# Kernel optimization log

Measured on AMD Instinct MI355X. Metric: run time of the kernel, lower is better.

The kernel has to match this reference:

```python
import jax, jax.numpy as jnp
import numpy as np

B, NOP, NMA = 16, 512, 64
D_OP, D_MA, D_EG = 16, 8, 8
HID, OUT = 256, 128
NEG_SLOPE = 0.2


def _mlp(x, w1, b1, w2, b2, w3, b3):
    # Linear -> ELU -> Linear -> ELU -> Linear (MLPs.project)
    h = jax.nn.elu(x @ w1 + b1)
    h = jax.nn.elu(h @ w2 + b2)
    return h @ w3 + b3


def _gatop(op, ma, eg, ma_adj, pre_adj, sub_adj, attn_pre, params):
    # params: list of 5 tuples (w1,b1,w2,b2,w3,b3) for gnn_layers[0..4]
    num = op.shape[1]
    # flag_ma=0 aggregation: adj[...,None]*op[:,None,:,:] summed over dim -2 == adj @ op
    pre_f1 = _mlp(jnp.einsum('bij,bjd->bid', pre_adj, op), *params[1])   # [B,NOP,OUT]
    sub_f1 = _mlp(jnp.einsum('bij,bjd->bid', sub_adj, op), *params[2])   # [B,NOP,OUT]
    self_f1 = _mlp(op, *params[3])  # identity adjacency -> aggregation is op itself
    # machine-edge features: [B,NOP,NMA,D_MA+D_EG]
    ma_eg = jnp.concatenate([ma_adj[..., None] * ma[:, None, :, :], eg], axis=-1)
    # flag_ma=1: mask then per-pair MLP -> [B,NOP,NMA,OUT]
    ma_f1 = _mlp(ma_adj[..., None] * ma_eg, *params[0])
    # flag_ma=2: mean over machines counting nonzero entries
    cnt = jnp.sum(ma_f1 != 0.0, axis=-2).astype(ma_f1.dtype)
    ma_f2 = _mlp(jnp.sum(ma_f1, axis=-2) / cnt, *params[4])              # [B,NOP,OUT]
    # NOTE: original code uses attn_pre for ALL four scores (faithful)
    att = lambda f: jnp.sum(f * attn_pre, axis=-1, keepdims=True)        # [B,NOP,1]
    pre_ut, sub_ut, self_ut, ma_ut = att(pre_f1), att(sub_f1), att(self_f1), att(ma_f2)
    lrelu = lambda x: jax.nn.leaky_relu(x, NEG_SLOPE)
    scores = jnp.concatenate([
        lrelu(pre_ut + self_ut), lrelu(sub_ut + self_ut),
        lrelu(self_ut + self_ut), lrelu(ma_ut + self_ut)], axis=1)       # [B,4*NOP,1]
    alpha = jax.nn.softmax(scores, axis=1)
    a_pre = alpha[:, :num]
    a_sub = alpha[:, num:2 * num]
    a_self = alpha[:, 2 * num:3 * num]
    a_ma = alpha[:, 3 * num:]
    return jax.nn.sigmoid(a_pre * pre_f1 + a_sub * sub_f1 + a_self * self_f1 + a_ma * ma_f2)


def setup_inputs() -> dict:
    key = jax.random.key(0)
    ks = jax.random.split(key, 40)
    inp = {
        'op': jax.random.normal(ks[0], (B, NOP, D_OP), jnp.float32),
        'ma': jax.random.normal(ks[1], (B, NMA, D_MA), jnp.float32),
        'eg': jax.random.normal(ks[2], (B, NOP, NMA, D_EG), jnp.float32),
        'op_ma_adj': jax.random.randint(ks[3], (B, NOP, NMA), 0, 2, jnp.int32),
        'op_pre_adj': jax.random.randint(ks[4], (B, NOP, NOP), 0, 2, jnp.int32),
        'op_sub_adj': jax.random.randint(ks[5], (B, NOP, NOP), 0, 2, jnp.int32),
        'batch_idxes': jnp.arange(B, dtype=jnp.int32),
        'attn_pre': jax.random.normal(ks[6], (1, 1, OUT), jnp.float32) * 0.1,
    }
    ins = [D_MA + D_EG, D_OP, D_OP, D_OP, OUT]
    k = 7
    for i, din in enumerate(ins):
        inp[f'm{i}_w1'] = jax.random.normal(ks[k], (din, HID), jnp.float32) / np.sqrt(din); k += 1
        inp[f'm{i}_b1'] = jnp.zeros((HID,), jnp.float32)
        inp[f'm{i}_w2'] = jax.random.normal(ks[k], (HID, HID), jnp.float32) / np.sqrt(HID); k += 1
        inp[f'm{i}_b2'] = jnp.zeros((HID,), jnp.float32)
        inp[f'm{i}_w3'] = jax.random.normal(ks[k], (HID, OUT), jnp.float32) / np.sqrt(HID); k += 1
        inp[f'm{i}_b3'] = jnp.zeros((OUT,), jnp.float32)
    return inp


def reference(op, ma, eg, op_ma_adj, op_pre_adj, op_sub_adj, batch_idxes, attn_pre,
              m0_w1, m0_b1, m0_w2, m0_b2, m0_w3, m0_b3,
              m1_w1, m1_b1, m1_w2, m1_b2, m1_w3, m1_b3,
              m2_w1, m2_b1, m2_w2, m2_b2, m2_w3, m2_b3,
              m3_w1, m3_b1, m3_w2, m3_b2, m3_w3, m3_b3,
              m4_w1, m4_b1, m4_w2, m4_b2, m4_w3, m4_b3):
    ma_adj = op_ma_adj[batch_idxes].astype(op.dtype)
    pre_adj = op_pre_adj[batch_idxes].astype(op.dtype)
    sub_adj = op_sub_adj[batch_idxes].astype(op.dtype)
    params = [
        (m0_w1, m0_b1, m0_w2, m0_b2, m0_w3, m0_b3),
        (m1_w1, m1_b1, m1_w2, m1_b2, m1_w3, m1_b3),
        (m2_w1, m2_b1, m2_w2, m2_b2, m2_w3, m2_b3),
        (m3_w1, m3_b1, m3_w2, m3_b2, m3_w3, m3_b3),
        (m4_w1, m4_b1, m4_w2, m4_b2, m4_w3, m4_b3),
    ]
    return _gatop(op, ma, eg, ma_adj, pre_adj, sub_adj, attn_pre, params)
```

## Files before the change

kernel.cpp:

```cpp
#include <hip/hip_runtime.h>
#include <math.h>

#define NBb  16
#define NOPc 512
#define NMAc 64
#define HIDc 256
#define OUTc 128
#define NROW (NBb * NOPc)
#define NEMAX (NROW * NMAc)

#define HX(row, col) ((col) ^ (8 * ((row) & 15)))
#define FX(row, col) ((col) ^ (4 * ((row) & 15)))

typedef unsigned int uint32;
typedef unsigned short ush;
typedef __attribute__((ext_vector_type(8))) short bf16x8;
typedef __attribute__((ext_vector_type(4))) float f32x4;

__device__ __forceinline__ ush f2bf(float v) {
    uint32 u = __float_as_uint(v);
    u += 0x7FFFu + ((u >> 16) & 1u);
    return (ush)(u >> 16);
}
__device__ __forceinline__ float bf2f(ush b) { return __uint_as_float(((uint32)b) << 16); }
__device__ __forceinline__ float eluf(float x) { return x > 0.f ? x : expm1f(x); }
__device__ __forceinline__ float eluf_fast(float x) { return x > 0.f ? x : __expf(x) - 1.f; }
__device__ __forceinline__ uint32 pkbf(float a, float b) {
    return __builtin_amdgcn_perm(__float_as_uint(b), __float_as_uint(a), 0x07060302u);
}
__device__ __forceinline__ uint32 pkbf_rne(float a, float b) {
    return (uint32)f2bf(a) | ((uint32)f2bf(b) << 16);
}
__device__ __forceinline__ void split2(float a, float b, uint32& hp, uint32& lp) {
    const uint32 ua = __float_as_uint(a), ub = __float_as_uint(b);
    hp = __builtin_amdgcn_perm(ub, ua, 0x07060302u);
    const float ra = a - __uint_as_float(ua & 0xFFFF0000u);
    const float rb = b - __uint_as_float(ub & 0xFFFF0000u);
    lp = __builtin_amdgcn_perm(__float_as_uint(rb), __float_as_uint(ra), 0x07060302u);
}
__device__ __forceinline__ uint32 pkadj(int a, int b) {
    return (a ? 0x3F80u : 0u) | (b ? 0x3F800000u : 0u);
}

#define MFMA(A, B, C) __builtin_amdgcn_mfma_f32_16x16x32_bf16((A), (B), (C), 0, 0, 0)

struct MlpPack {
    const ush *w1h, *w1l, *w2h, *w2l, *w3h, *w3l;
    const float *b1, *b2, *b3;
};

__device__ __forceinline__ void mlp3_core32(
    const MlpPack& P, const int KB1,
    const ush* Xh, const ush* Xl, ush* Hh, ush* Hl, f32x4 acc3[2][2])
{
    const int tid = threadIdx.x;
    const int wv = tid >> 6, lane = tid & 63, r = lane & 15, g = lane >> 4;
    const int KX = KB1 * 32;

    {
        f32x4 acc[4][2];
        #pragma unroll
        for (int a = 0; a < 4; ++a) {
            const float4 bv = *(const float4*)(P.b1 + (wv * 4 + a) * 16 + 4 * g);
            #pragma unroll
            for (int m = 0; m < 2; ++m) acc[a][m] = f32x4{bv.x, bv.y, bv.z, bv.w};
        }
        #pragma unroll 1
        for (int kb = 0; kb < KB1; ++kb) {
            bf16x8 wh[4], wl[4];
            #pragma unroll
            for (int a = 0; a < 4; ++a) {
                const size_t o = ((size_t)(kb * 16 + (wv * 4 + a)) * 64 + lane) * 8;
                wh[a] = *(const bf16x8*)(P.w1h + o);
                wl[a] = *(const bf16x8*)(P.w1l + o);
            }
            #pragma unroll
            for (int m = 0; m < 2; ++m) {
                const int row = 16 * m + r;
                const int ki = kb * 32 + 8 * g;
                bf16x8 xh = *(const bf16x8*)(Xh + row * KX + ki);
                bf16x8 xl = *(const bf16x8*)(Xl + row * KX + ki);
                #pragma unroll
                for (int a = 0; a < 4; ++a) {
                    acc[a][m] = MFMA(wh[a], xh, acc[a][m]);
                    acc[a][m] = MFMA(wh[a], xl, acc[a][m]);
                    acc[a][m] = MFMA(wl[a], xh, acc[a][m]);
                }
            }
        }
        #pragma unroll
        for (int a = 0; a < 4; ++a) {
            const int n0 = (wv * 4 + a) * 16 + 4 * g;
            #pragma unroll
            for (int m = 0; m < 2; ++m) {
                const int row = 16 * m + r;
                const float y0 = eluf_fast(acc[a][m][0]);
                const float y1 = eluf_fast(acc[a][m][1]);
                const float y2 = eluf_fast(acc[a][m][2]);
                const float y3 = eluf_fast(acc[a][m][3]);
                uint2 uh, ul;
                split2(y0, y1, uh.x, ul.x);
                split2(y2, y3, uh.y, ul.y);
                const int idx = row * 256 + HX(row, n0);
                *(uint2*)(Hh + idx) = uh;
                *(uint2*)(Hl + idx) = ul;
            }
        }
    }
    __syncthreads();

    {
        f32x4 acc[4][2];
        #pragma unroll
        for (int a = 0; a < 4; ++a) {
            const float4 bv = *(const float4*)(P.b2 + (wv * 4 + a) * 16 + 4 * g);
            #pragma unroll
            for (int m = 0; m < 2; ++m) acc[a][m] = f32x4{bv.x, bv.y, bv.z, bv.w};
        }
        #pragma unroll 1
        for (int kb = 0; kb < 8; ++kb) {
            bf16x8 wh[4], wl[4];
            #pragma unroll
            for (int a = 0; a < 4; ++a) {
                const size_t o = ((size_t)(kb * 16 + (wv * 4 + a)) * 64 + lane) * 8;
                wh[a] = *(const bf16x8*)(P.w2h + o);
                wl[a] = *(const bf16x8*)(P.w2l + o);
            }
            #pragma unroll
            for (int m = 0; m < 2; ++m) {
                const int row = 16 * m + r;
                const int k0 = kb * 32 + 8 * g;
                const int idx = row * 256 + HX(row, k0);
                bf16x8 hh = *(const bf16x8*)(Hh + idx);
                bf16x8 hl = *(const bf16x8*)(Hl + idx);
                #pragma unroll
                for (int a = 0; a < 4; ++a) {
                    acc[a][m] = MFMA(wh[a], hh, acc[a][m]);
                    acc[a][m] = MFMA(wh[a], hl, acc[a][m]);
                    acc[a][m] = MFMA(wl[a], hh, acc[a][m]);
                }
            }
        }
        __syncthreads();
        #pragma unroll
        for (int a = 0; a < 4; ++a) {
            const int n0 = (wv * 4 + a) * 16 + 4 * g;
            #pragma unroll
            for (int m = 0; m < 2; ++m) {
                const int row = 16 * m + r;
                const float y0 = eluf_fast(acc[a][m][0]);
                const float y1 = eluf_fast(acc[a][m][1]);
                const float y2 = eluf_fast(acc[a][m][2]);
                const float y3 = eluf_fast(acc[a][m][3]);
                uint2 uh, ul;
                split2(y0, y1, uh.x, ul.x);
                split2(y2, y3, uh.y, ul.y);
                const int idx = row * 256 + HX(row, n0);
                *(uint2*)(Hh + idx) = uh;
                *(uint2*)(Hl + idx) = ul;
            }
        }
    }
    __syncthreads();

    {
        #pragma unroll
        for (int a = 0; a < 2; ++a) {
            const float4 bv = *(const float4*)(P.b3 + (wv * 2 + a) * 16 + 4 * g);
            #pragma unroll
            for (int m = 0; m < 2; ++m) acc3[a][m] = f32x4{bv.x, bv.y, bv.z, bv.w};
        }
        #pragma unroll 1
        for (int kb = 0; kb < 8; ++kb) {
            bf16x8 wh[2], wl[2];
            #pragma unroll
            for (int a = 0; a < 2; ++a) {
                const size_t o = ((size_t)(kb * 8 + (wv * 2 + a)) * 64 + lane) * 8;
                wh[a] = *(const bf16x8*)(P.w3h + o);
                wl[a] = *(const bf16x8*)(P.w3l + o);
            }
            #pragma unroll
            for (int m = 0; m < 2; ++m) {
                const int row = 16 * m + r;
                const int k0 = kb * 32 + 8 * g;
                const int idx = row * 256 + HX(row, k0);
                bf16x8 hh = *(const bf16x8*)(Hh + idx);
                bf16x8 hl = *(const bf16x8*)(Hl + idx);
                #pragma unroll
                for (int a = 0; a < 2; ++a) {
                    acc3[a][m] = MFMA(wh[a], hh, acc3[a][m]);
                    acc3[a][m] = MFMA(wh[a], hl, acc3[a][m]);
                    acc3[a][m] = MFMA(wl[a], hh, acc3[a][m]);
                }
            }
        }
    }
}

__global__ __launch_bounds__(256) void count_kernel(const int* __restrict__ ma_adj,
                                                    const int* __restrict__ bidx,
                                                    int* __restrict__ counts)
{
    const int tid = threadIdx.x;
    const int rid = blockIdx.x * 4 + (tid >> 6);
    const int lane = tid & 63;
    const int b = rid >> 9, i = rid & 511;
    const int bi = bidx[b];
    const int active = (ma_adj[((size_t)bi * NOPc + i) * NMAc + lane] != 0) ? 1 : 0;
    const unsigned long long mk = __ballot(active);
    if (lane == 0) counts[rid] = (int)__popcll(mk);
}

__global__ __launch_bounds__(1024) void scan_kernel(const int* __restrict__ counts,
                                                    int* __restrict__ bases,
                                                    int* __restrict__ natot,
                                                    ush* __restrict__ Xq,
                                                    ush* __restrict__ rowseg)
{
    __shared__ int tot[1024];
    const int t = threadIdx.x;
    int loc[8];
    int s = 0;
    #pragma unroll
    for (int k = 0; k < 8; ++k) { loc[k] = s; s += counts[t * 8 + k]; }
    tot[t] = s;
    __syncthreads();
    for (int off = 1; off < 1024; off <<= 1) {
        const int v = (t >= off) ? tot[t - off] : 0;
        __syncthreads();
        tot[t] += v;
        __syncthreads();
    }
    const int base = tot[t] - s;
    #pragma unroll
    for (int k = 0; k < 8; ++k) bases[t * 8 + k] = base + loc[k];
    const int NA = tot[1023];
    if (t == 0) *natot = NA;
    __syncthreads();
    const int NApad = (NA + 63) & ~63;
    for (int idx = NA * 16 + t; idx < NApad * 16; idx += 1024) Xq[idx] = 0;
    for (int idx = NA + t; idx < NApad; idx += 1024) rowseg[idx] = (ush)0xFFFFu;
}

struct PackDesc { const float* src; ush* dh; ush* dl; int kreal; int kbn; int nbn; };
struct PrepArgs {
    PackDesc d[15];
    const float* op; const int* pre_adj; const int* sub_adj; const int* ma_adj;
    const int* bidx;
    float* pre_agg; float* sub_agg;
    const float *z_b1, *z_w2, *z_b2, *z_w3, *z_b3;
    float* f1z;
    const float* ma; const float* eg; const int* bases;
    ush* Xq; ush* rowseg; float* sumG;
};

__global__ __launch_bounds__(256) void prep_kernel(PrepArgs A)
{
    __shared__ float shmem[8192];
    const int blk = blockIdx.x;
    const int t = threadIdx.x;
    if (blk < 960) {
        const PackDesc d = A.d[blk >> 6];
        const int sub = blk & 63;
        const int total = d.kbn * d.nbn * 512;
        const int N = d.nbn * 16;
        for (int idx = sub * 256 + t; idx < total; idx += 64 * 256) {
            const int e = idx & 7;
            const int l = (idx >> 3) & 63;
            const int t2 = idx >> 9;
            const int nb = t2 % d.nbn;
            const int kb = t2 / d.nbn;
            const int k = kb * 32 + ((l >> 4) << 3) + e;
            const int n = nb * 16 + (l & 15);
            const float v = (k < d.kreal) ? d.src[(size_t)k * N + n] : 0.f;
            const ush hi = f2bf(v);
            d.dh[idx] = hi;
            d.dl[idx] = f2bf(v - bf2f(hi));
        }
    } else if (blk < 1088) {
        const int e = blk - 960;
        const int b = e >> 3;
        const int i0 = (e & 7) * 64;
        const int bi = A.bidx[b];
        ush* opH = (ush*)shmem;
        ush* opL = opH + 8192;
        for (int idx = t; idx < 8192; idx += 256) {
            const int j = idx >> 4, dd = idx & 15;
            const float v = A.op[(size_t)b * 8192 + idx];
            const int kb = j >> 5, gg = (j >> 3) & 3, ee = j & 7;
            const int di = ((kb * 64 + gg * 16 + dd) << 3) + ee;
            const uint32 uv = __float_as_uint(v);
            opH[di] = (ush)(uv >> 16);
            const float rest = v - __uint_as_float(uv & 0xFFFF0000u);
            opL[di] = (ush)(__float_as_uint(rest) >> 16);
        }
        __syncthreads();
        const int wv = t >> 6, lane = t & 63, r = lane & 15, g = lane >> 4;
        const int i = i0 + wv * 16 + r;
        const int4* pr4 = (const int4*)(A.pre_adj + ((size_t)bi * NOPc + i) * NOPc);
        const int4* sr4 = (const int4*)(A.sub_adj + ((size_t)bi * NOPc + i) * NOPc);
        f32x4 accP = {0.f, 0.f, 0.f, 0.f}, accS = {0.f, 0.f, 0.f, 0.f};
        #pragma unroll 2
        for (int kb = 0; kb < 16; ++kb) {
            const int jo = kb * 8 + 2 * g;
            const int4 p0 = pr4[jo], p1 = pr4[jo + 1];
            const int4 s0 = sr4[jo], s1 = sr4[jo + 1];
            bf16x8 ap, as;
            {
                uint32 u0 = pkadj(p0.x, p0.y), u1 = pkadj(p0.z, p0.w);
                uint32 u2 = pkadj(p1.x, p1.y), u3 = pkadj(p1.z, p1.w);
                uint32* pa = (uint32*)&ap;
                pa[0] = u0; pa[1] = u1; pa[2] = u2; pa[3] = u3;
            }
            {
                uint32 u0 = pkadj(s0.x, s0.y), u1 = pkadj(s0.z, s0.w);
                uint32 u2 = pkadj(s1.x, s1.y), u3 = pkadj(s1.z, s1.w);
                uint32* pa = (uint32*)&as;
                pa[0] = u0; pa[1] = u1; pa[2] = u2; pa[3] = u3;
            }
            const bf16x8 oh = *(const bf16x8*)(opH + ((kb * 64 + lane) << 3));
            const bf16x8 ol = *(const bf16x8*)(opL + ((kb * 64 + lane) << 3));
            accP = MFMA(oh, ap, accP);
            accP = MFMA(ol, ap, accP);
            accS = MFMA(oh, as, accS);
            accS = MFMA(ol, as, accS);
        }
        float4 vp, vs;
        vp.x = accP[0]; vp.y = accP[1]; vp.z = accP[2]; vp.w = accP[3];
        vs.x = accS[0]; vs.y = accS[1]; vs.z = accS[2]; vs.w = accS[3];
        *(float4*)&A.pre_agg[((size_t)b * NOPc + i) * 16 + 4 * g] = vp;
        *(float4*)&A.sub_agg[((size_t)b * NOPc + i) * 16 + 4 * g] = vs;
    } else if (blk == 1088) {
        shmem[t] = eluf(A.z_b1[t]);
        __syncthreads();
        float acc = A.z_b2[t];
        for (int k = 0; k < 256; ++k) acc += shmem[k] * A.z_w2[(size_t)k * 256 + t];
        __syncthreads();
        shmem[256 + t] = eluf(acc);
        __syncthreads();
        if (t < 128) {
            float a = A.z_b3[t];
            for (int k = 0; k < 256; ++k) a += shmem[256 + k] * A.z_w3[(size_t)k * 128 + t];
            A.f1z[t] = a;
        }
    } else {
        const int rid = (blk - 1089) * 4 + (t >> 6);
        const int lane = t & 63;
        const int b = rid >> 9, i = rid & 511;
        const int bi = A.bidx[b];
        const int act = (A.ma_adj[((size_t)bi * NOPc + i) * NMAc + lane] != 0) ? 1 : 0;
        const unsigned long long mk = __ballot(act);
        if (act) {
            const int pos = A.bases[rid] + (int)__popcll(mk & ((1ull << lane) - 1ull));
            const float4* mp = (const float4*)(A.ma + ((size_t)b * NMAc + lane) * 8);
            const float4* ep = (const float4*)(A.eg + (((size_t)b * NOPc + i) * NMAc + lane) * 8);
            const float4 m0 = mp[0], m1 = mp[1], e0 = ep[0], e1 = ep[1];
            uint4 u0, u1;
            u0.x = pkbf_rne(m0.x, m0.y); u0.y = pkbf_rne(m0.z, m0.w);
            u0.z = pkbf_rne(m1.x, m1.y); u0.w = pkbf_rne(m1.z, m1.w);
            u1.x = pkbf_rne(e0.x, e0.y); u1.y = pkbf_rne(e0.z, e0.w);
            u1.z = pkbf_rne(e1.x, e1.y); u1.w = pkbf_rne(e1.z, e1.w);
            uint4* dst = (uint4*)(A.Xq + (size_t)pos * 16);
            dst[0] = u0;
            dst[1] = u1;
            A.rowseg[pos] = (ush)rid;
        }
        A.sumG[(size_t)rid * 128 + lane] = 0.f;
        A.sumG[(size_t)rid * 128 + 64 + lane] = 0.f;
    }
}

struct EF1Args {
    const ush* Xq; const ush* rowseg; const int* natot; MlpPack P0;
    float* sumG;
    const float* X[3]; MlpPack P[3]; float* f1[3]; float* ut[3];
};

__global__ __launch_bounds__(256, 4) void edge_f1_kernel(EF1Args A, const float* __restrict__ attn)
{
    __shared__ unsigned char smem[36992];
    const int blk = blockIdx.x;
    const int tid = threadIdx.x;
    const int wv = tid >> 6, lane = tid & 63, r = lane & 15, g = lane >> 4;

    if (blk < 8192) {
        const int NA = *A.natot;
        const int tile = blk;
        if (tile * 64 >= NA) return;
        ush* Hh = (ush*)smem;
        ush* segid = (ush*)(smem + 32768);
        const MlpPack& P = A.P0;
        if (tid < 64) segid[tid] = A.rowseg[(size_t)tile * 64 + tid];

        {
            f32x4 acc[4][4];
            #pragma unroll
            for (int a = 0; a < 4; ++a) {
                const float4 bv = *(const float4*)(P.b1 + (wv * 4 + a) * 16 + 4 * g);
                #pragma unroll
                for (int m = 0; m < 4; ++m) acc[a][m] = f32x4{bv.x, bv.y, bv.z, bv.w};
            }
            bf16x8 wh[4];
            #pragma unroll
            for (int a = 0; a < 4; ++a)
                wh[a] = *(const bf16x8*)(P.w1h + ((size_t)(wv * 4 + a) * 64 + lane) * 8);
            #pragma unroll
            for (int m = 0; m < 4; ++m) {
                const int gr = tile * 64 + 16 * m + r;
                bf16x8 xh = {0, 0, 0, 0, 0, 0, 0, 0};
                if (g < 2) xh = *(const bf16x8*)(A.Xq + (size_t)gr * 16 + 8 * g);
                #pragma unroll
                for (int a = 0; a < 4; ++a) acc[a][m] = MFMA(wh[a], xh, acc[a][m]);
            }
            #pragma unroll
            for (int a = 0; a < 4; ++a) {
                const int n0 = (wv * 4 + a) * 16 + 4 * g;
                #pragma unroll
                for (int m = 0; m < 4; ++m) {
                    const int row = 16 * m + r;
                    const float y0 = eluf_fast(acc[a][m][0]);
                    const float y1 = eluf_fast(acc[a][m][1]);
                    const float y2 = eluf_fast(acc[a][m][2]);
                    const float y3 = eluf_fast(acc[a][m][3]);
                    uint2 u; u.x = pkbf(y0, y1); u.y = pkbf(y2, y3);
                    *(uint2*)(Hh + row * 256 + HX(row, n0)) = u;
                }
            }
        }
        __syncthreads();

        {
            f32x4 acc[4][4];
            #pragma unroll
            for (int a = 0; a < 4; ++a) {
                const float4 bv = *(const float4*)(P.b2 + (wv * 4 + a) * 16 + 4 * g);
                #pragma unroll
                for (int m = 0; m < 4; ++m) acc[a][m] = f32x4{bv.x, bv.y, bv.z, bv.w};
            }
            #pragma unroll 1
            for (int kb = 0; kb < 8; ++kb) {
                bf16x8 wh[4];
                #pragma unroll
                for (int a = 0; a < 4; ++a)
                    wh[a] = *(const bf16x8*)(P.w2h + ((size_t)(kb * 16 + (wv * 4 + a)) * 64 + lane) * 8);
                #pragma unroll
                for (int m = 0; m < 4; ++m) {
                    const int row = 16 * m + r;
                    const int k0 = kb * 32 + 8 * g;
                    bf16x8 hh = *(const bf16x8*)(Hh + row * 256 + HX(row, k0));
                    #pragma unroll
                    for (int a = 0; a < 4; ++a) acc[a][m] = MFMA(wh[a], hh, acc[a][m]);
                }
            }
            __syncthreads();
            #pragma unroll
            for (int a = 0; a < 4; ++a) {
                const int n0 = (wv * 4 + a) * 16 + 4 * g;
                #pragma unroll
                for (int m = 0; m < 4; ++m) {
                    const int row = 16 * m + r;
                    const float y0 = eluf_fast(acc[a][m][0]);
                    const float y1 = eluf_fast(acc[a][m][1]);
                    const float y2 = eluf_fast(acc[a][m][2]);
                    const float y3 = eluf_fast(acc[a][m][3]);
                    uint2 u; u.x = pkbf(y0, y1); u.y = pkbf(y2, y3);
                    *(uint2*)(Hh + row * 256 + HX(row, n0)) = u;
                }
            }
        }
        __syncthreads();

        f32x4 acc3[2][4];
        #pragma unroll
        for (int a = 0; a < 2; ++a) {
            const float4 bv = *(const float4*)(P.b3 + (wv * 2 + a) * 16 + 4 * g);
            #pragma unroll
            for (int m = 0; m < 4; ++m) acc3[a][m] = f32x4{bv.x, bv.y, bv.z, bv.w};
        }
        #pragma unroll 1
        for (int kb = 0; kb < 8; ++kb) {
            bf16x8 wh[2];
            #pragma unroll
            for (int a = 0; a < 2; ++a)
                wh[a] = *(const bf16x8*)(P.w3h + ((size_t)(kb * 8 + (wv * 2 + a)) * 64 + lane) * 8);
            #pragma unroll
            for (int m = 0; m < 4; ++m) {
                const int row = 16 * m + r;
                const int k0 = kb * 32 + 8 * g;
                bf16x8 hh = *(const bf16x8*)(Hh + row * 256 + HX(row, k0));
                #pragma unroll
                for (int a = 0; a < 2; ++a) acc3[a][m] = MFMA(wh[a], hh, acc3[a][m]);
            }
        }
        __syncthreads();

        float* f1buf = (float*)Hh;
        #pragma unroll
        for (int a = 0; a < 2; ++a) {
            const int n0 = (wv * 2 + a) * 16 + 4 * g;
            #pragma unroll
            for (int m = 0; m < 4; ++m) {
                const int row = 16 * m + r;
                float4 y;
                y.x = acc3[a][m][0];
                y.y = acc3[a][m][1];
                y.z = acc3[a][m][2];
                y.w = acc3[a][m][3];
                *(float4*)&f1buf[row * 128 + FX(row, n0)] = y;
            }
        }
        __syncthreads();

        {
            const int c = tid & 127, h = tid >> 7;
            const int r0p = h * 32;
            float accS = 0.f;
            int cur = -1;
            #pragma unroll
            for (int j = 0; j < 32; ++j) {
                const int rl = r0p + j;
                const int sg = (int)segid[rl];
                if (sg != cur) {
                    if ((unsigned)cur < (unsigned)NROW)
                        atomicAdd(&A.sumG[(size_t)cur * 128 + c], accS);
                    cur = sg; accS = 0.f;
                }
                accS += f1buf[rl * 128 + FX(rl, c)];
            }
            if ((unsigned)cur < (unsigned)NROW)
                atomicAdd(&A.sumG[(size_t)cur * 128 + c], accS);
        }
    } else {
        const int pb = blk - 8192;
        const int p = pb >> 8;
        const int row0 = (pb & 255) * 32;
        ush* Xh = (ush*)smem;
        ush* Xl = (ush*)(smem + 2048);
        ush* Hh = (ush*)(smem + 4096);
        ush* Hl = (ush*)(smem + 20480);
        float* UT = (float*)(smem + 36864);
        const float* Xg = A.X[p];
        const MlpPack P = A.P[p];
        float* f1_out = A.f1[p];
        float* ut_out = A.ut[p];
        if (tid < 32) UT[tid] = 0.f;
        for (int idx = tid; idx < 32 * 32; idx += 256) {
            const int row = idx >> 5, k = idx & 31;
            float v = 0.f;
            if (k < 16) v = Xg[(size_t)(row0 + row) * 16 + k];
            const uint32 uv = __float_as_uint(v);
            Xh[idx] = (ush)(uv >> 16);
            const float rest = v - __uint_as_float(uv & 0xFFFF0000u);
            Xl[idx] = (ush)(__float_as_uint(rest) >> 16);
        }
        __syncthreads();
        f32x4 acc3[2][2];
        mlp3_core32(P, 1, Xh, Xl, Hh, Hl, acc3);

        float utp[2] = {0.f, 0.f};
        #pragma unroll
        for (int a = 0; a < 2; ++a) {
            const int n0 = (wv * 2 + a) * 16 + 4 * g;
            const float4 av = *(const float4*)(attn + n0);
            #pragma unroll
            for (int m = 0; m < 2; ++m) {
                float4 y;
                y.x = acc3[a][m][0];
                y.y = acc3[a][m][1];
                y.z = acc3[a][m][2];
                y.w = acc3[a][m][3];
                *(float4*)&f1_out[(size_t)(row0 + 16 * m + r) * OUTc + n0] = y;
                utp[m] += y.x * av.x + y.y * av.y + y.z * av.z + y.w * av.w;
            }
        }
        #pragma unroll
        for (int m = 0; m < 2; ++m) {
            float v = utp[m];
            v += __shfl_xor(v, 16);
            v += __shfl_xor(v, 32);
            if (lane < 16) atomicAdd(&UT[16 * m + r], v);
        }
        __syncthreads();
        if (tid < 32) ut_out[row0 + tid] = UT[tid];
    }
}

__global__ __launch_bounds__(256, 3) void p3_kernel(
    MlpPack P, const float* __restrict__ attn,
    const float* __restrict__ sumG,
    const int* __restrict__ counts, const float* __restrict__ f1z,
    float* __restrict__ f1_out, float* __restrict__ ut_out)
{
    __shared__ ush Xh[32 * 128], Xl[32 * 128];
    __shared__ ush Hh[32 * 256], Hl[32 * 256];
    __shared__ float UT[32];
    const int tid = threadIdx.x;
    const int row0 = blockIdx.x * 32;
    if (tid < 32) UT[tid] = 0.f;
    for (int idx = tid; idx < 32 * 128; idx += 256) {
        const int row = idx >> 7, k = idx & 127;
        const size_t rid = (size_t)(row0 + row);
        const float na = (float)counts[rid];
        const float nz = 64.f - na;
        const float fz = f1z[k];
        const float v = (sumG[rid * 128 + k] + nz * fz)
                      / (na + nz * ((fz != 0.f) ? 1.f : 0.f));
        const uint32 uv = __float_as_uint(v);
        Xh[idx] = (ush)(uv >> 16);
        const float rest = v - __uint_as_float(uv & 0xFFFF0000u);
        Xl[idx] = (ush)(__float_as_uint(rest) >> 16);
    }
    __syncthreads();
    f32x4 acc3[2][2];
    mlp3_core32(P, 4, Xh, Xl, Hh, Hl, acc3);

    const int wv = tid >> 6, lane = tid & 63, r = lane & 15, g = lane >> 4;
    float utp[2] = {0.f, 0.f};
    #pragma unroll
    for (int a = 0; a < 2; ++a) {
        const int n0 = (wv * 2 + a) * 16 + 4 * g;
        const float4 av = *(const float4*)(attn + n0);
        #pragma unroll
        for (int m = 0; m < 2; ++m) {
            float4 y;
            y.x = acc3[a][m][0];
            y.y = acc3[a][m][1];
            y.z = acc3[a][m][2];
            y.w = acc3[a][m][3];
            *(float4*)&f1_out[(size_t)(row0 + 16 * m + r) * OUTc + n0] = y;
            utp[m] += y.x * av.x + y.y * av.y + y.z * av.z + y.w * av.w;
        }
    }
    #pragma unroll
    for (int m = 0; m < 2; ++m) {
        float v = utp[m];
        v += __shfl_xor(v, 16);
        v += __shfl_xor(v, 32);
        if (lane < 16) atomicAdd(&UT[16 * m + r], v);
    }
    __syncthreads();
    if (tid < 32) ut_out[row0 + tid] = UT[tid];
}

__global__ __launch_bounds__(256) void combine2_kernel(
    const float* __restrict__ uts,
    const float* __restrict__ pre_f1, const float* __restrict__ sub_f1,
    const float* __restrict__ self_f1, const float* __restrict__ ma_f2,
    float* __restrict__ out)
{
    __shared__ float sc[4 * NOPc];
    __shared__ float red[256];
    const int b = blockIdx.x >> 4, chunk = blockIdx.x & 15;
    const int t = threadIdx.x;
    const float* put = uts + 0 * NROW + (size_t)b * NOPc;
    const float* sut = uts + 1 * NROW + (size_t)b * NOPc;
    const float* eut = uts + 2 * NROW + (size_t)b * NOPc;
    const float* mut = uts + 3 * NROW + (size_t)b * NOPc;
    for (int i = t; i < NOPc; i += 256) {
        const float se = eut[i];
        const float s0 = put[i] + se, s1 = sut[i] + se, s2 = se + se, s3 = mut[i] + se;
        sc[0 * NOPc + i] = s0 > 0.f ? s0 : 0.2f * s0;
        sc[1 * NOPc + i] = s1 > 0.f ? s1 : 0.2f * s1;
        sc[2 * NOPc + i] = s2 > 0.f ? s2 : 0.2f * s2;
        sc[3 * NOPc + i] = s3 > 0.f ? s3 : 0.2f * s3;
    }
    __syncthreads();
    float mx = -INFINITY;
    for (int idx = t; idx < 4 * NOPc; idx += 256) mx = fmaxf(mx, sc[idx]);
    red[t] = mx;
    __syncthreads();
    for (int s = 128; s > 0; s >>= 1) { if (t < s) red[t] = fmaxf(red[t], red[t + s]); __syncthreads(); }
    mx = red[0];
    __syncthreads();
    float ps = 0.f;
    for (int idx = t; idx < 4 * NOPc; idx += 256) {
        const float e = expf(sc[idx] - mx);
        sc[idx] = e;
        ps += e;
    }
    red[t] = ps;
    __syncthreads();
    for (int s = 128; s > 0; s >>= 1) { if (t < s) red[t] += red[t + s]; __syncthreads(); }
    const float invZ = 1.f / red[0];

    const size_t base4 = (size_t)b * 16384 + (size_t)chunk * 1024;
    #pragma unroll
    for (int k = 0; k < 4; ++k) {
        const size_t e4 = base4 + k * 256 + t;
        const int i = (int)((e4 >> 5) & 511);
        const float a0 = sc[0 * NOPc + i] * invZ;
        const float a1 = sc[1 * NOPc + i] * invZ;
        const float a2 = sc[2 * NOPc + i] * invZ;
        const float a3 = sc[3 * NOPc + i] * invZ;
        const float4 vp = ((const float4*)pre_f1)[e4];
        const float4 vs = ((const float4*)sub_f1)[e4];
        const float4 ve = ((const float4*)self_f1)[e4];
        const float4 vm = ((const float4*)ma_f2)[e4];
        float4 o;
        o.x = 1.f / (1.f + expf(-(a0 * vp.x + a1 * vs.x + a2 * ve.x + a3 * vm.x)));
        o.y = 1.f / (1.f + expf(-(a0 * vp.y + a1 * vs.y + a2 * ve.y + a3 * vm.y)));
        o.z = 1.f / (1.f + expf(-(a0 * vp.z + a1 * vs.z + a2 * ve.z + a3 * vm.z)));
        o.w = 1.f / (1.f + expf(-(a0 * vp.w + a1 * vs.w + a2 * ve.w + a3 * vm.w)));
        ((float4*)out)[e4] = o;
    }
}

extern "C" void kernel_launch(void* const* d_in, const int* in_sizes, int n_in,
                              void* d_out, int out_size, void* d_ws, size_t ws_size,
                              hipStream_t stream) {
    const float* op      = (const float*)d_in[0];
    const float* ma      = (const float*)d_in[1];
    const float* eg      = (const float*)d_in[2];
    const int*   ma_adj  = (const int*)d_in[3];
    const int*   pre_adj = (const int*)d_in[4];
    const int*   sub_adj = (const int*)d_in[5];
    const int*   bidx    = (const int*)d_in[6];
    const float* attn    = (const float*)d_in[7];
    float* out = (float*)d_out;
    const float* Wraw[5][6];
    for (int m = 0; m < 5; ++m)
        for (int j = 0; j < 6; ++j)
            Wraw[m][j] = (const float*)d_in[8 + 6 * m + j];

    float* wsf = (float*)d_ws;
    float* pre_agg = wsf;  wsf += (size_t)NROW * 16;
    float* sub_agg = wsf;  wsf += (size_t)NROW * 16;
    float* pre_f1  = wsf;  wsf += (size_t)NROW * OUTc;
    float* sub_f1  = wsf;  wsf += (size_t)NROW * OUTc;
    float* self_f1 = wsf;  wsf += (size_t)NROW * OUTc;
    float* ma_f2   = wsf;  wsf += (size_t)NROW * OUTc;
    float* uts     = wsf;  wsf += (size_t)4 * NROW;
    float* f1z     = wsf;  wsf += 128;
    float* sumG    = wsf;  wsf += (size_t)NROW * 128;
    int*   counts  = (int*)wsf;   wsf += NROW;
    int*   bases   = (int*)wsf;   wsf += NROW;
    int*   natot   = (int*)wsf;   wsf += 16;
    ush*   rowseg  = (ush*)wsf;   wsf += NEMAX / 2;
    ush*   Xq      = (ush*)wsf;   wsf += (size_t)NEMAX * 8;
    ush*   packp   = (ush*)wsf;

    PrepArgs pa;
    MlpPack pk[5];
    for (int m = 0; m < 5; ++m) {
        const int kre[3] = { (m == 4 ? 128 : 16), 256, 256 };
        const int kbn[3] = { (m == 4 ? 4 : 1), 8, 8 };
        const int nbn[3] = { 16, 16, 8 };
        const ush* dh[3]; const ush* dl[3];
        for (int j = 0; j < 3; ++j) {
            const int id = m * 3 + j;
            pa.d[id].src = Wraw[m][2 * j];
            pa.d[id].kreal = kre[j];
            pa.d[id].kbn = kbn[j];
            pa.d[id].nbn = nbn[j];
            const int cnt = kbn[j] * nbn[j] * 512;
            pa.d[id].dh = packp; dh[j] = packp; packp += cnt;
            pa.d[id].dl = packp; dl[j] = packp; packp += cnt;
        }
        pk[m].w1h = dh[0]; pk[m].w1l = dl[0];
        pk[m].w2h = dh[1]; pk[m].w2l = dl[1];
        pk[m].w3h = dh[2]; pk[m].w3l = dl[2];
        pk[m].b1 = Wraw[m][1]; pk[m].b2 = Wraw[m][3]; pk[m].b3 = Wraw[m][5];
    }
    pa.op = op; pa.pre_adj = pre_adj; pa.sub_adj = sub_adj; pa.ma_adj = ma_adj;
    pa.bidx = bidx;
    pa.pre_agg = pre_agg; pa.sub_agg = sub_agg;
    pa.z_b1 = Wraw[0][1]; pa.z_w2 = Wraw[0][2]; pa.z_b2 = Wraw[0][3];
    pa.z_w3 = Wraw[0][4]; pa.z_b3 = Wraw[0][5];
    pa.f1z = f1z;
    pa.ma = ma; pa.eg = eg; pa.bases = bases;
    pa.Xq = Xq; pa.rowseg = rowseg; pa.sumG = sumG;

    EF1Args ea;
    ea.Xq = Xq; ea.rowseg = rowseg; ea.natot = natot; ea.P0 = pk[0];
    ea.sumG = sumG;
    ea.X[0] = pre_agg; ea.X[1] = sub_agg; ea.X[2] = op;
    ea.P[0] = pk[1];   ea.P[1] = pk[2];   ea.P[2] = pk[3];
    ea.f1[0] = pre_f1; ea.f1[1] = sub_f1; ea.f1[2] = self_f1;
    ea.ut[0] = uts + 0 * NROW;
    ea.ut[1] = uts + 1 * NROW;
    ea.ut[2] = uts + 2 * NROW;

    count_kernel<<<dim3(NROW / 4), 256, 0, stream>>>(ma_adj, bidx, counts);
    scan_kernel<<<1, 1024, 0, stream>>>(counts, bases, natot, Xq, rowseg);
    prep_kernel<<<dim3(960 + 128 + 1 + NROW / 4), 256, 0, stream>>>(pa);
    edge_f1_kernel<<<dim3(8192 + 768), 256, 0, stream>>>(ea, attn);
    p3_kernel<<<dim3(256), 256, 0, stream>>>(pk[4], attn, sumG, counts, f1z,
                                             ma_f2, uts + 3 * NROW);
    combine2_kernel<<<dim3(NBb * 16), 256, 0, stream>>>(uts, pre_f1, sub_f1, self_f1, ma_f2, out);
}
```

Measured before the change: 147.7 us.

## Raise parallelism in tail kernels and schedule node MLP blocks first

The shared MLP core is templated on the number of 16-row tiles, so p3_kernel can process 16 rows per block instead of 32. That doubles its grid to 512 blocks and lowers per-block shared memory, and launch bounds are raised to 4 blocks per SM. combine2 likewise uses 32 chunks per batch, twice as many blocks each doing half the work. In edge_f1_kernel the 768 node-MLP blocks now take the low block indices so they are dispatched before the edge tiles. The aim is better GPU fill in the small tail kernels and less tail imbalance. The cost is weights reloaded more often per row in p3, and the softmax statistics recomputed by twice as many combine blocks.

```diff
diff --git a/kernel.cpp b/kernel.cpp
--- a/kernel.cpp
+++ b/kernel.cpp
@@ -49,21 +49,22 @@
     const float *b1, *b2, *b3;
 };
 
-__device__ __forceinline__ void mlp3_core32(
+template<int M>
+__device__ __forceinline__ void mlp3_coreM(
     const MlpPack& P, const int KB1,
-    const ush* Xh, const ush* Xl, ush* Hh, ush* Hl, f32x4 acc3[2][2])
+    const ush* Xh, const ush* Xl, ush* Hh, ush* Hl, f32x4 acc3[2][M])
 {
     const int tid = threadIdx.x;
     const int wv = tid >> 6, lane = tid & 63, r = lane & 15, g = lane >> 4;
     const int KX = KB1 * 32;
 
     {
-        f32x4 acc[4][2];
+        f32x4 acc[4][M];
         #pragma unroll
         for (int a = 0; a < 4; ++a) {
             const float4 bv = *(const float4*)(P.b1 + (wv * 4 + a) * 16 + 4 * g);
             #pragma unroll
-            for (int m = 0; m < 2; ++m) acc[a][m] = f32x4{bv.x, bv.y, bv.z, bv.w};
+            for (int m = 0; m < M; ++m) acc[a][m] = f32x4{bv.x, bv.y, bv.z, bv.w};
         }
         #pragma unroll 1
         for (int kb = 0; kb < KB1; ++kb) {
@@ -75,7 +76,7 @@
                 wl[a] = *(const bf16x8*)(P.w1l + o);
             }
             #pragma unroll
-            for (int m = 0; m < 2; ++m) {
+            for (int m = 0; m < M; ++m) {
                 const int row = 16 * m + r;
                 const int ki = kb * 32 + 8 * g;
                 bf16x8 xh = *(const bf16x8*)(Xh + row * KX + ki);
@@ -92,7 +93,7 @@
         for (int a = 0; a < 4; ++a) {
             const int n0 = (wv * 4 + a) * 16 + 4 * g;
             #pragma unroll
-            for (int m = 0; m < 2; ++m) {
+            for (int m = 0; m < M; ++m) {
                 const int row = 16 * m + r;
                 const float y0 = eluf_fast(acc[a][m][0]);
                 const float y1 = eluf_fast(acc[a][m][1]);
@@ -110,12 +111,12 @@
     __syncthreads();
 
     {
-        f32x4 acc[4][2];
+        f32x4 acc[4][M];
         #pragma unroll
         for (int a = 0; a < 4; ++a) {
             const float4 bv = *(const float4*)(P.b2 + (wv * 4 + a) * 16 + 4 * g);
             #pragma unroll
-            for (int m = 0; m < 2; ++m) acc[a][m] = f32x4{bv.x, bv.y, bv.z, bv.w};
+            for (int m = 0; m < M; ++m) acc[a][m] = f32x4{bv.x, bv.y, bv.z, bv.w};
         }
         #pragma unroll 1
         for (int kb = 0; kb < 8; ++kb) {
@@ -127,7 +128,7 @@
                 wl[a] = *(const bf16x8*)(P.w2l + o);
             }
             #pragma unroll
-            for (int m = 0; m < 2; ++m) {
+            for (int m = 0; m < M; ++m) {
                 const int row = 16 * m + r;
                 const int k0 = kb * 32 + 8 * g;
                 const int idx = row * 256 + HX(row, k0);
@@ -146,7 +147,7 @@
         for (int a = 0; a < 4; ++a) {
             const int n0 = (wv * 4 + a) * 16 + 4 * g;
             #pragma unroll
-            for (int m = 0; m < 2; ++m) {
+            for (int m = 0; m < M; ++m) {
                 const int row = 16 * m + r;
                 const float y0 = eluf_fast(acc[a][m][0]);
                 const float y1 = eluf_fast(acc[a][m][1]);
@@ -168,7 +169,7 @@
         for (int a = 0; a < 2; ++a) {
             const float4 bv = *(const float4*)(P.b3 + (wv * 2 + a) * 16 + 4 * g);
             #pragma unroll
-            for (int m = 0; m < 2; ++m) acc3[a][m] = f32x4{bv.x, bv.y, bv.z, bv.w};
+            for (int m = 0; m < M; ++m) acc3[a][m] = f32x4{bv.x, bv.y, bv.z, bv.w};
         }
         #pragma unroll 1
         for (int kb = 0; kb < 8; ++kb) {
@@ -180,7 +181,7 @@
                 wl[a] = *(const bf16x8*)(P.w3l + o);
             }
             #pragma unroll
-            for (int m = 0; m < 2; ++m) {
+            for (int m = 0; m < M; ++m) {
                 const int row = 16 * m + r;
                 const int k0 = kb * 32 + 8 * g;
                 const int idx = row * 256 + HX(row, k0);
@@ -383,9 +384,9 @@
     const int tid = threadIdx.x;
     const int wv = tid >> 6, lane = tid & 63, r = lane & 15, g = lane >> 4;
 
-    if (blk < 8192) {
+    if (blk >= 768) {
         const int NA = *A.natot;
-        const int tile = blk;
+        const int tile = blk - 768;
         if (tile * 64 >= NA) return;
         ush* Hh = (ush*)smem;
         ush* segid = (ush*)(smem + 32768);
@@ -531,7 +532,7 @@
                 atomicAdd(&A.sumG[(size_t)cur * 128 + c], accS);
         }
     } else {
-        const int pb = blk - 8192;
+        const int pb = blk;
         const int p = pb >> 8;
         const int row0 = (pb & 255) * 32;
         ush* Xh = (ush*)smem;
@@ -555,7 +556,7 @@
         }
         __syncthreads();
         f32x4 acc3[2][2];
-        mlp3_core32(P, 1, Xh, Xl, Hh, Hl, acc3);
+        mlp3_coreM<2>(P, 1, Xh, Xl, Hh, Hl, acc3);
 
         float utp[2] = {0.f, 0.f};
         #pragma unroll
@@ -585,19 +586,19 @@
     }
 }
 
-__global__ __launch_bounds__(256, 3) void p3_kernel(
+__global__ __launch_bounds__(256, 4) void p3_kernel(
     MlpPack P, const float* __restrict__ attn,
     const float* __restrict__ sumG,
     const int* __restrict__ counts, const float* __restrict__ f1z,
     float* __restrict__ f1_out, float* __restrict__ ut_out)
 {
-    __shared__ ush Xh[32 * 128], Xl[32 * 128];
-    __shared__ ush Hh[32 * 256], Hl[32 * 256];
-    __shared__ float UT[32];
+    __shared__ ush Xh[16 * 128], Xl[16 * 128];
+    __shared__ ush Hh[16 * 256], Hl[16 * 256];
+    __shared__ float UT[16];
     const int tid = threadIdx.x;
-    const int row0 = blockIdx.x * 32;
-    if (tid < 32) UT[tid] = 0.f;
-    for (int idx = tid; idx < 32 * 128; idx += 256) {
+    const int row0 = blockIdx.x * 16;
+    if (tid < 16) UT[tid] = 0.f;
+    for (int idx = tid; idx < 16 * 128; idx += 256) {
         const int row = idx >> 7, k = idx & 127;
         const size_t rid = (size_t)(row0 + row);
         const float na = (float)counts[rid];
@@ -611,35 +612,31 @@
         Xl[idx] = (ush)(__float_as_uint(rest) >> 16);
     }
     __syncthreads();
-    f32x4 acc3[2][2];
-    mlp3_core32(P, 4, Xh, Xl, Hh, Hl, acc3);
+    f32x4 acc3[2][1];
+    mlp3_coreM<1>(P, 4, Xh, Xl, Hh, Hl, acc3);
 
     const int wv = tid >> 6, lane = tid & 63, r = lane & 15, g = lane >> 4;
-    float utp[2] = {0.f, 0.f};
+    float utp = 0.f;
     #pragma unroll
     for (int a = 0; a < 2; ++a) {
         const int n0 = (wv * 2 + a) * 16 + 4 * g;
         const float4 av = *(const float4*)(attn + n0);
-        #pragma unroll
-        for (int m = 0; m < 2; ++m) {
-            float4 y;
-            y.x = acc3[a][m][0];
-            y.y = acc3[a][m][1];
-            y.z = acc3[a][m][2];
-            y.w = acc3[a][m][3];
-            *(float4*)&f1_out[(size_t)(row0 + 16 * m + r) * OUTc + n0] = y;
-            utp[m] += y.x * av.x + y.y * av.y + y.z * av.z + y.w * av.w;
-        }
-    }
-    #pragma unroll
-    for (int m = 0; m < 2; ++m) {
-        float v = utp[m];
+        float4 y;
+        y.x = acc3[a][0][0];
+        y.y = acc3[a][0][1];
+        y.z = acc3[a][0][2];
+        y.w = acc3[a][0][3];
+        *(float4*)&f1_out[(size_t)(row0 + r) * OUTc + n0] = y;
+        utp += y.x * av.x + y.y * av.y + y.z * av.z + y.w * av.w;
+    }
+    {
+        float v = utp;
         v += __shfl_xor(v, 16);
         v += __shfl_xor(v, 32);
-        if (lane < 16) atomicAdd(&UT[16 * m + r], v);
-    }
-    __syncthreads();
-    if (tid < 32) ut_out[row0 + tid] = UT[tid];
+        if (lane < 16) atomicAdd(&UT[r], v);
+    }
+    __syncthreads();
+    if (tid < 16) ut_out[row0 + tid] = UT[tid];
 }
 
 __global__ __launch_bounds__(256) void combine2_kernel(
@@ -650,7 +647,7 @@
 {
     __shared__ float sc[4 * NOPc];
     __shared__ float red[256];
-    const int b = blockIdx.x >> 4, chunk = blockIdx.x & 15;
+    const int b = blockIdx.x >> 5, chunk = blockIdx.x & 31;
     const int t = threadIdx.x;
     const float* put = uts + 0 * NROW + (size_t)b * NOPc;
     const float* sut = uts + 1 * NROW + (size_t)b * NOPc;
@@ -683,9 +680,9 @@
     for (int s = 128; s > 0; s >>= 1) { if (t < s) red[t] += red[t + s]; __syncthreads(); }
     const float invZ = 1.f / red[0];
 
-    const size_t base4 = (size_t)b * 16384 + (size_t)chunk * 1024;
+    const size_t base4 = (size_t)b * 16384 + (size_t)chunk * 512;
     #pragma unroll
-    for (int k = 0; k < 4; ++k) {
+    for (int k = 0; k < 2; ++k) {
         const size_t e4 = base4 + k * 256 + t;
         const int i = (int)((e4 >> 5) & 511);
         const float a0 = sc[0 * NOPc + i] * invZ;
@@ -783,8 +780,8 @@
     count_kernel<<<dim3(NROW / 4), 256, 0, stream>>>(ma_adj, bidx, counts);
     scan_kernel<<<1, 1024, 0, stream>>>(counts, bases, natot, Xq, rowseg);
     prep_kernel<<<dim3(960 + 128 + 1 + NROW / 4), 256, 0, stream>>>(pa);
-    edge_f1_kernel<<<dim3(8192 + 768), 256, 0, stream>>>(ea, attn);
-    p3_kernel<<<dim3(256), 256, 0, stream>>>(pk[4], attn, sumG, counts, f1z,
+    edge_f1_kernel<<<dim3(768 + 8192), 256, 0, stream>>>(ea, attn);
+    p3_kernel<<<dim3(512), 256, 0, stream>>>(pk[4], attn, sumG, counts, f1z,
                                              ma_f2, uts + 3 * NROW);
-    combine2_kernel<<<dim3(NBb * 16), 256, 0, stream>>>(uts, pre_f1, sub_f1, self_f1, ma_f2, out);
-}
+    combine2_kernel<<<dim3(NBb * 32), 256, 0, stream>>>(uts, pre_f1, sub_f1, self_f1, ma_f2, out);
+}
```

New measurement: 148.5 us. About the same (+0.5%).
